# Performance work log

Measured on AMD Instinct MI355X. Metric: run time of the kernel, lower is better.

The kernel has to match this reference:

```python
import jax, jax.numpy as jnp
import numpy as np

B, S, L, H, D, FF, V = 2, 1024, 12, 12, 768, 3072, 50265
DH = D // H
W1 = 256                      # one-sided window (attention_window=512)
MOTIF = (31 + 96 + 80) * 2    # 414
MAXPOS = 4098
EPS = 1e-5
NEG = jnp.float32(-1e9)


def _ln(x, s, b):
    m = jnp.mean(x, -1, keepdims=True)
    v = jnp.mean(jnp.square(x - m), -1, keepdims=True)
    return (x - m) * jax.lax.rsqrt(v + EPS) * s + b


def setup_inputs() -> dict:
    key = jax.random.key(0)
    ks = iter(jax.random.split(key, 48))
    n = lambda *sh: jax.random.normal(next(ks), sh, jnp.float32) * 0.02
    return {
        "input_ids": jax.random.randint(next(ks), (B, S), 0, V),
        "attention_mask": jnp.ones((B, S), jnp.int32),
        "motif_dist": jax.random.uniform(next(ks), (B, MOTIF), dtype=jnp.float32),
        "emb_word": n(V, D), "emb_pos": n(MAXPOS, D), "emb_type": n(1, D),
        "emb_ln_s": jnp.ones((D,)), "emb_ln_b": jnp.zeros((D,)),
        "Wq": n(L, D, D), "bq": jnp.zeros((L, D)),
        "Wk": n(L, D, D), "bk": jnp.zeros((L, D)),
        "Wv": n(L, D, D), "bv": jnp.zeros((L, D)),
        "Wqg": n(L, D, D), "bqg": jnp.zeros((L, D)),
        "Wkg": n(L, D, D), "bkg": jnp.zeros((L, D)),
        "Wvg": n(L, D, D), "bvg": jnp.zeros((L, D)),
        "Wo": n(L, D, D), "bo": jnp.zeros((L, D)),
        "ln1_s": jnp.ones((L, D)), "ln1_b": jnp.zeros((L, D)),
        "Wi": n(L, D, FF), "bi": jnp.zeros((L, FF)),
        "Wo2": n(L, FF, D), "bo2": jnp.zeros((L, D)),
        "ln2_s": jnp.ones((L, D)), "ln2_b": jnp.zeros((L, D)),
        "head_Wd": n(D + MOTIF, D), "head_bd": jnp.zeros((D,)),
        "head_Wp": n(D, 2), "head_bp": jnp.zeros((2,)),
    }


def reference(input_ids, attention_mask, motif_dist, emb_word, emb_pos, emb_type,
              emb_ln_s, emb_ln_b, Wq, bq, Wk, bk, Wv, bv, Wqg, bqg, Wkg, bkg,
              Wvg, bvg, Wo, bo, ln1_s, ln1_b, Wi, bi, Wo2, bo2, ln2_s, ln2_b,
              head_Wd, head_bd, head_Wp, head_bp):
    Bn, Sn = input_ids.shape
    scale = 1.0 / np.sqrt(DH)
    # RoBERTa-style embeddings: positions start at padding_idx+1 = 2
    pos_ids = jnp.arange(Sn) + 2
    x = emb_word[input_ids] + emb_pos[pos_ids][None] + emb_type[0][None, None]
    x = _ln(x, emb_ln_s, emb_ln_b)

    key_valid = attention_mask.astype(bool)[:, None, None, :]      # [B,1,1,S]
    idx = jnp.arange(Sn)
    is_global = idx == 0                                           # default: CLS-only global
    band = jnp.abs(idx[:, None] - idx[None, :]) <= W1
    # local query attends to its sliding window plus all global keys
    local_allowed = (band | is_global[None, :])[None, None] & key_valid

    def heads(t, s):
        return t.reshape(Bn, s, H, DH).transpose(0, 2, 1, 3)       # [B,H,s,DH]

    for l in range(L):
        q = heads(x @ Wq[l] + bq[l], Sn) * scale
        k = heads(x @ Wk[l] + bk[l], Sn)
        v = heads(x @ Wv[l] + bv[l], Sn)
        scores = jnp.einsum('bhid,bhjd->bhij', q, k)
        probs = jax.nn.softmax(jnp.where(local_allowed, scores, NEG), -1)
        out = jnp.einsum('bhij,bhjd->bhid', probs, v)              # [B,H,S,DH]
        # global (CLS) query: full attention using the *_global projections
        qg = heads(x[:, :1] @ Wqg[l] + bqg[l], 1) * scale          # [B,H,1,DH]
        kg = heads(x @ Wkg[l] + bkg[l], Sn)
        vg = heads(x @ Wvg[l] + bvg[l], Sn)
        sg = jnp.einsum('bhid,bhjd->bhij', qg, kg)                 # [B,H,1,S]
        pg = jax.nn.softmax(jnp.where(key_valid, sg, NEG), -1)
        og = jnp.einsum('bhij,bhjd->bhid', pg, vg)                 # [B,H,1,DH]
        out = jnp.concatenate([og, out[:, :, 1:]], axis=2)
        out = out.transpose(0, 2, 1, 3).reshape(Bn, Sn, D)
        x = _ln(x + out @ Wo[l] + bo[l], ln1_s[l], ln1_b[l])
        h = jax.nn.gelu(x @ Wi[l] + bi[l], approximate=False)
        x = _ln(x + h @ Wo2[l] + bo2[l], ln2_s[l], ln2_b[l])

    # classification head: CLS hidden state concat motif distribution
    hcat = jnp.concatenate([x[:, 0, :], motif_dist], axis=-1)
    return jnp.tanh(hcat @ head_Wd + head_bd) @ head_Wp + head_bp
```

## Files before the change

### kernel.cpp

```cpp
#include <hip/hip_runtime.h>
#include <math.h>

typedef unsigned short u16;
typedef __attribute__((ext_vector_type(8))) short short8;
typedef __attribute__((ext_vector_type(4))) float f32x4;

#define BB 2
#define SS 1024
#define LL 12
#define HH 12
#define DD 768
#define FFF 3072
#define MOTIF 414
#define HCAT (DD + MOTIF)
#define W1 256
#define NEGV -1e9f
#define EPS 1e-5f
#define SCALE 0.125f
#define LD5 3840
#define WL_ELE 8257536

__device__ __forceinline__ float bf2f(u16 u) {
    union { unsigned i; float f; } x; x.i = ((unsigned)u) << 16; return x.f;
}
__device__ __forceinline__ u16 f2bf(float f) {
    union { float f; unsigned i; } x; x.f = f;
    unsigned r = x.i + 0x7fffu + ((x.i >> 16) & 1u);
    return (u16)(r >> 16);
}

__device__ __forceinline__ void gld16(const u16* g, u16* l) {
    __builtin_amdgcn_global_load_lds((const __attribute__((address_space(1))) void*)g,
                                     (__attribute__((address_space(3))) void*)l, 16, 0, 0);
}

__device__ __forceinline__ float block_reduce_sum(float v, float* red) {
    int t = threadIdx.x;
    red[t] = v; __syncthreads();
    #pragma unroll
    for (int s = 128; s > 0; s >>= 1) {
        if (t < s) red[t] += red[t + s];
        __syncthreads();
    }
    float r = red[0]; __syncthreads();
    return r;
}

__global__ __launch_bounds__(256) void embed_ln_kernel(
    const int* __restrict__ ids, const float* __restrict__ ew,
    const float* __restrict__ ep, const float* __restrict__ et,
    const float* __restrict__ gs, const float* __restrict__ gb,
    float* __restrict__ X, u16* __restrict__ Xb) {
    __shared__ float red[256];
    int row = blockIdx.x;
    int s = row % SS;
    int id = ids[row];
    int t = threadIdx.x;
    float v[3];
    float sum = 0.f;
    #pragma unroll
    for (int i = 0; i < 3; ++i) {
        int d = t + 256 * i;
        float x = ew[(size_t)id * DD + d] + ep[(size_t)(s + 2) * DD + d] + et[d];
        v[i] = x; sum += x;
    }
    sum = block_reduce_sum(sum, red);
    float m = sum * (1.f / DD);
    float sq = 0.f;
    #pragma unroll
    for (int i = 0; i < 3; ++i) { float c = v[i] - m; sq += c * c; }
    sq = block_reduce_sum(sq, red);
    float inv = rsqrtf(sq * (1.f / DD) + EPS);
    #pragma unroll
    for (int i = 0; i < 3; ++i) {
        int d = t + 256 * i;
        float o = (v[i] - m) * inv * gs[d] + gb[d];
        X[(size_t)row * DD + d] = o;
        Xb[(size_t)row * DD + d] = f2bf(o);
    }
}

__global__ __launch_bounds__(256) void add_ln_kernel(
    float* __restrict__ X, u16* __restrict__ Xb,
    const float* __restrict__ T1, const float* __restrict__ T2, int useT2,
    const float* __restrict__ gs, const float* __restrict__ gb) {
    __shared__ float red[256];
    int row = blockIdx.x;
    int t = threadIdx.x;
    float v[3];
    float sum = 0.f;
    #pragma unroll
    for (int i = 0; i < 3; ++i) {
        int d = t + 256 * i;
        size_t idx = (size_t)row * DD + d;
        float x = X[idx] + T1[idx] + (useT2 ? T2[idx] : 0.f);
        v[i] = x; sum += x;
    }
    sum = block_reduce_sum(sum, red);
    float m = sum * (1.f / DD);
    float sq = 0.f;
    #pragma unroll
    for (int i = 0; i < 3; ++i) { float c = v[i] - m; sq += c * c; }
    sq = block_reduce_sum(sq, red);
    float inv = rsqrtf(sq * (1.f / DD) + EPS);
    #pragma unroll
    for (int i = 0; i < 3; ++i) {
        int d = t + 256 * i;
        float o = (v[i] - m) * inv * gs[d] + gb[d];
        X[(size_t)row * DD + d] = o;
        Xb[(size_t)row * DD + d] = f2bf(o);
    }
}

template <int LAYERED>
__global__ __launch_bounds__(256) void conv_all_kernel(
    const float* __restrict__ Wqp, const float* __restrict__ Wkp,
    const float* __restrict__ Wvp, const float* __restrict__ Wkgp,
    const float* __restrict__ Wvgp, const float* __restrict__ Wop,
    const float* __restrict__ Wip, const float* __restrict__ Wo2p,
    u16* __restrict__ WtBase) {
    __shared__ float Tt[32][33];
    int l = LAYERED ? blockIdx.y : 0;
    size_t oDD = (size_t)l * DD * DD;
    size_t oFF = (size_t)l * DD * FFF;
    u16* Wt6  = WtBase + (size_t)l * WL_ELE;
    u16* Wti  = Wt6 + 6 * DD * DD;
    u16* Wto2 = Wti + FFF * DD;
    int tid = blockIdx.x;
    const float* W; u16* Wt; int Nd, Kd, n0, k0;
    if (tid < 3456) {
        int z = tid / 576, rem = tid % 576;
        const float* w6[6] = {Wqp + oDD, Wkp + oDD, Wvp + oDD, Wkgp + oDD, Wvgp + oDD, Wop + oDD};
        W = w6[z];
        Wt = Wt6 + (size_t)z * DD * DD;
        Nd = DD; Kd = DD; n0 = (rem % 24) * 32; k0 = (rem / 24) * 32;
    } else if (tid < 5760) {
        int i = tid - 3456;
        W = Wip + oFF; Wt = Wti; Nd = FFF; Kd = DD; n0 = (i % 96) * 32; k0 = (i / 96) * 32;
    } else {
        int i = tid - 5760;
        W = Wo2p + oFF; Wt = Wto2; Nd = DD; Kd = FFF; n0 = (i % 24) * 32; k0 = (i / 24) * 32;
    }
    int t = threadIdx.x;
    int r = t >> 3, c = (t & 7) * 4;
    float4 v = *(const float4*)(W + (size_t)(k0 + r) * Nd + n0 + c);
    Tt[r][c] = v.x; Tt[r][c + 1] = v.y; Tt[r][c + 2] = v.z; Tt[r][c + 3] = v.w;
    __syncthreads();
    int n = t >> 3, k4 = (t & 7) * 4;
    unsigned lo = (unsigned)f2bf(Tt[k4][n])     | ((unsigned)f2bf(Tt[k4 + 1][n]) << 16);
    unsigned hi = (unsigned)f2bf(Tt[k4 + 2][n]) | ((unsigned)f2bf(Tt[k4 + 3][n]) << 16);
    uint2 wv; wv.x = lo; wv.y = hi;
    *(uint2*)&Wt[(size_t)(n0 + n) * Kd + k0 + k4] = wv;
}

__global__ __launch_bounds__(256) void bcat_kernel(
    const float* __restrict__ bq, const float* __restrict__ bk,
    const float* __restrict__ bv, const float* __restrict__ bkg,
    const float* __restrict__ bvg, float* __restrict__ bcat) {
    int tid = blockIdx.x * 256 + threadIdx.x;
    if (tid >= LL * LD5) return;
    int l = tid / LD5, r = tid % LD5, z = r / DD, j = r % DD;
    const float* src = (z == 0) ? bq : (z == 1) ? bk : (z == 2) ? bv : (z == 3) ? bkg : bvg;
    bcat[tid] = src[l * DD + j];
}

template <int ACT, int OBF>
__global__ __launch_bounds__(256) void gemm_bf16(
    const u16* __restrict__ A, const u16* __restrict__ Bt,
    const float* __restrict__ bias, void* __restrict__ C0, void* __restrict__ C1,
    int M, int N, int K, int Ksplit) {
    __shared__ __align__(16) u16 As[128 * 32];
    __shared__ __align__(16) u16 Bs[128 * 32];
    int z = blockIdx.z;
    int kbeg = z * Ksplit;
    int kend = kbeg + Ksplit; if (kend > K) kend = K;
    void* Cout = z ? C1 : C0;
    int t = threadIdx.x, lane = t & 63, wv = t >> 6;
    int bm = blockIdx.y * 128, bn = blockIdx.x * 128;
    int wm = wv >> 1, wn = wv & 1;
    int h = lane >> 4, q15 = lane & 15;
    f32x4 acc[4][4];
    #pragma unroll
    for (int i = 0; i < 4; ++i)
        #pragma unroll
        for (int j = 0; j < 4; ++j) { acc[i][j][0] = 0.f; acc[i][j][1] = 0.f; acc[i][j][2] = 0.f; acc[i][j][3] = 0.f; }

    for (int k0 = kbeg; k0 < kend; k0 += 32) {
        #pragma unroll
        for (int op = 0; op < 2; ++op) {
            int rc = wv * 32 + op * 16;
            int r = rc + (lane >> 2), s = lane & 3;
            gld16(A  + (size_t)(bm + r) * K + k0 + ((s ^ (r & 3)) * 8), &As[rc * 32]);
            gld16(Bt + (size_t)(bn + r) * K + k0 + ((s ^ (r & 3)) * 8), &Bs[rc * 32]);
        }
        __syncthreads();
        short8 af[4], bfr[4];
        #pragma unroll
        for (int mf = 0; mf < 4; ++mf) {
            int row = wm * 64 + mf * 16 + q15;
            af[mf] = *(const short8*)&As[row * 32 + ((h ^ (row & 3)) * 8)];
        }
        #pragma unroll
        for (int nf = 0; nf < 4; ++nf) {
            int row = wn * 64 + nf * 16 + q15;
            bfr[nf] = *(const short8*)&Bs[row * 32 + ((h ^ (row & 3)) * 8)];
        }
        #pragma unroll
        for (int mf = 0; mf < 4; ++mf)
            #pragma unroll
            for (int nf = 0; nf < 4; ++nf)
                acc[mf][nf] = __builtin_amdgcn_mfma_f32_16x16x32_bf16(af[mf], bfr[nf], acc[mf][nf], 0, 0, 0);
        __syncthreads();
    }
    float* Cf = (float*)Cout;
    u16*   Cb = (u16*)Cout;
    #pragma unroll
    for (int mf = 0; mf < 4; ++mf) {
        int mbase = bm + wm * 64 + mf * 16 + h * 4;
        #pragma unroll
        for (int nf = 0; nf < 4; ++nf) {
            int n = bn + wn * 64 + nf * 16 + q15;
            float bv = 0.f;
            if (z == 0) bv = bias[n];
            #pragma unroll
            for (int rg = 0; rg < 4; ++rg) {
                float val = acc[mf][nf][rg] + bv;
                if (ACT == 1) val = 0.5f * val * (1.f + erff(val * 0.70710678118654752f));
                if (OBF) Cb[(size_t)(mbase + rg) * N + n] = f2bf(val);
                else     Cf[(size_t)(mbase + rg) * N + n] = val;
            }
        }
    }
}

__global__ __launch_bounds__(256) void attn_local_mfma(
    const u16* __restrict__ QKV, const int* __restrict__ mask,
    u16* __restrict__ AO) {
    __shared__ __align__(16) u16 Qs[64 * 64];
    __shared__ __align__(16) u16 Ks[64 * 64];
    __shared__ __align__(16) u16 Vst[64 * 64];
    __shared__ __align__(16) u16 Pld[4][16 * 64];
    __shared__ float msk[64];
    int bid = blockIdx.x;
    int qt = bid & 15;
    int hh = (bid >> 4) % HH;
    int b  = bid / (16 * HH);
    int t = threadIdx.x, lane = t & 63, wv = t >> 6;
    int h = lane >> 4, q15 = lane & 15;
    int i0 = qt * 64;

    #pragma unroll
    for (int op = 0; op < 2; ++op) {
        int r = wv * 16 + op * 8 + (lane >> 3), s = lane & 7;
        gld16(QKV + (size_t)(b * SS + i0 + r) * LD5 + hh * 64 + ((s ^ (r & 7)) * 8),
              &Qs[(wv * 16 + op * 8) * 64]);
    }
    __syncthreads();
    short8 bq[2];
    {
        int qrow = wv * 16 + q15;
        #pragma unroll
        for (int ks = 0; ks < 2; ++ks)
            bq[ks] = *(const short8*)&Qs[qrow * 64 + (((ks * 4 + h) ^ (qrow & 7)) * 8)];
    }

    float mrun = -3e38f, lrun = 0.f;
    f32x4 o[4];
    #pragma unroll
    for (int nf = 0; nf < 4; ++nf) { o[nf][0] = 0.f; o[nf][1] = 0.f; o[nf][2] = 0.f; o[nf][3] = 0.f; }

    int jlo = i0 - W1; if (jlo < 0) jlo = 0;
    int jend = i0 + 64 + W1; if (jend > SS) jend = SS;
    int hasCLS = (jlo > 0) ? 1 : 0;
    int nt = hasCLS + (jend - jlo) / 64;
    int iq = i0 + wv * 16 + q15;

    for (int tt = 0; tt < nt; ++tt) {
        int base = (hasCLS && tt == 0) ? 0 : jlo + (tt - hasCLS) * 64;
        if (tt > 0) __syncthreads();
        #pragma unroll
        for (int op = 0; op < 2; ++op) {
            int r = wv * 16 + op * 8 + (lane >> 3), s = lane & 7;
            gld16(QKV + (size_t)(b * SS + base + r) * LD5 + 768 + hh * 64 + ((s ^ (r & 7)) * 8),
                  &Ks[(wv * 16 + op * 8) * 64]);
        }
        {
            int k2 = t & 31, dsec = t >> 5;
            const u16* vp = QKV + (size_t)(b * SS + base + 2 * k2) * LD5 + 1536 + hh * 64 + dsec * 8;
            union { uint4 v; u16 e[8]; } r0, r1;
            r0.v = *(const uint4*)vp;
            r1.v = *(const uint4*)(vp + LD5);
            int slot = k2 >> 2;
            #pragma unroll
            for (int j = 0; j < 8; ++j) {
                int d = dsec * 8 + j;
                unsigned val = (unsigned)r0.e[j] | ((unsigned)r1.e[j] << 16);
                *(unsigned*)&Vst[d * 64 + ((slot ^ (d & 7)) * 8) + ((2 * k2) & 7)] = val;
            }
        }
        if (t < 64) msk[t] = (float)mask[b * SS + base + t];
        __syncthreads();

        f32x4 sacc[4];
        #pragma unroll
        for (int kf = 0; kf < 4; ++kf) { sacc[kf][0] = 0.f; sacc[kf][1] = 0.f; sacc[kf][2] = 0.f; sacc[kf][3] = 0.f; }
        #pragma unroll
        for (int ks = 0; ks < 2; ++ks) {
            #pragma unroll
            for (int kf = 0; kf < 4; ++kf) {
                int krow = kf * 16 + q15;
                short8 afr = *(const short8*)&Ks[krow * 64 + (((ks * 4 + h) ^ (krow & 7)) * 8)];
                sacc[kf] = __builtin_amdgcn_mfma_f32_16x16x32_bf16(afr, bq[ks], sacc[kf], 0, 0, 0);
            }
        }
        float pv[4][4];
        float tmax = -3e38f;
        #pragma unroll
        for (int kf = 0; kf < 4; ++kf) {
            #pragma unroll
            for (int rg = 0; rg < 4; ++rg) {
                int kl = kf * 16 + h * 4 + rg;
                int key = base + kl;
                int dj = iq - key; int adj = dj < 0 ? -dj : dj;
                bool valid = ((adj <= W1) || (key == 0)) && (msk[kl] != 0.f);
                float s = valid ? sacc[kf][rg] * SCALE : NEGV;
                pv[kf][rg] = s;
                tmax = fmaxf(tmax, s);
            }
        }
        tmax = fmaxf(tmax, __shfl_xor(tmax, 16));
        tmax = fmaxf(tmax, __shfl_xor(tmax, 32));
        float mnew = fmaxf(mrun, tmax);
        float fac = __expf(mrun - mnew);
        mrun = mnew;
        float psum = 0.f;
        #pragma unroll
        for (int kf = 0; kf < 4; ++kf)
            #pragma unroll
            for (int rg = 0; rg < 4; ++rg) {
                float p = __expf(pv[kf][rg] - mnew);
                pv[kf][rg] = p; psum += p;
            }
        psum += __shfl_xor(psum, 16);
        psum += __shfl_xor(psum, 32);
        lrun = lrun * fac + psum;
        #pragma unroll
        for (int kf = 0; kf < 4; ++kf) {
            unsigned lo = (unsigned)f2bf(pv[kf][0]) | ((unsigned)f2bf(pv[kf][1]) << 16);
            unsigned hi = (unsigned)f2bf(pv[kf][2]) | ((unsigned)f2bf(pv[kf][3]) << 16);
            int slot = 2 * kf + (h >> 1);
            uint2 w; w.x = lo; w.y = hi;
            *(uint2*)&Pld[wv][q15 * 64 + ((slot ^ (q15 & 7)) * 8) + 4 * (h & 1)] = w;
        }
        float fo0 = __shfl(fac, (h * 4 + 0) | (lane & 48));
        float fo1 = __shfl(fac, (h * 4 + 1) | (lane & 48));
        float fo2 = __shfl(fac, (h * 4 + 2) | (lane & 48));
        float fo3 = __shfl(fac, (h * 4 + 3) | (lane & 48));
        #pragma unroll
        for (int nf = 0; nf < 4; ++nf) {
            o[nf][0] *= fo0; o[nf][1] *= fo1; o[nf][2] *= fo2; o[nf][3] *= fo3;
        }
        asm volatile("s_waitcnt lgkmcnt(0)" ::: "memory");
        #pragma unroll
        for (int ks = 0; ks < 2; ++ks) {
            short8 ap = *(const short8*)&Pld[wv][q15 * 64 + (((ks * 4 + h) ^ (q15 & 7)) * 8)];
            #pragma unroll
            for (int nf = 0; nf < 4; ++nf) {
                int d = nf * 16 + q15;
                short8 bvf = *(const short8*)&Vst[d * 64 + (((ks * 4 + h) ^ (d & 7)) * 8)];
                o[nf] = __builtin_amdgcn_mfma_f32_16x16x32_bf16(ap, bvf, o[nf], 0, 0, 0);
            }
        }
    }
    float linv = 1.f / lrun;
    float g0 = __shfl(linv, (h * 4 + 0) | (lane & 48));
    float g1 = __shfl(linv, (h * 4 + 1) | (lane & 48));
    float g2 = __shfl(linv, (h * 4 + 2) | (lane & 48));
    float g3 = __shfl(linv, (h * 4 + 3) | (lane & 48));
    size_t rb = (size_t)(b * SS + i0 + wv * 16 + h * 4);
    #pragma unroll
    for (int nf = 0; nf < 4; ++nf) {
        int d = hh * 64 + nf * 16 + q15;
        AO[(rb + 0) * DD + d] = f2bf(o[nf][0] * g0);
        AO[(rb + 1) * DD + d] = f2bf(o[nf][1] * g1);
        AO[(rb + 2) * DD + d] = f2bf(o[nf][2] * g2);
        AO[(rb + 3) * DD + d] = f2bf(o[nf][3] * g3);
    }
}

__global__ __launch_bounds__(512) void attn_global_kernel(
    const float* __restrict__ Xf, const float* __restrict__ Wqg,
    const float* __restrict__ bqg, const u16* __restrict__ QKV,
    const int* __restrict__ mask, u16* __restrict__ AO) {
    __shared__ float x0[DD];
    __shared__ float qv[64];
    __shared__ float sc[SS];
    __shared__ float red[512];
    __shared__ float part[8][64];
    int b = blockIdx.x / HH, hh = blockIdx.x % HH;
    int t = threadIdx.x;
    for (int i = t; i < DD; i += 512) x0[i] = Xf[(size_t)b * SS * DD + i];
    __syncthreads();
    {
        int d = t & 63, p = t >> 6;
        float acc = 0.f;
        int k0 = p * 96;
        #pragma unroll 8
        for (int k = k0; k < k0 + 96; ++k)
            acc += x0[k] * Wqg[(size_t)k * DD + hh * 64 + d];
        part[p][d] = acc;
    }
    __syncthreads();
    if (t < 64) {
        float s = bqg[hh * 64 + t];
        #pragma unroll
        for (int p = 0; p < 8; ++p) s += part[p][t];
        qv[t] = s * SCALE;
    }
    __syncthreads();
    for (int j = t; j < SS; j += 512) {
        const u16* kp = QKV + (size_t)(b * SS + j) * LD5 + 2304 + hh * 64;
        float acc = 0.f;
        #pragma unroll
        for (int d0 = 0; d0 < 64; d0 += 8) {
            union { uint4 v; u16 e[8]; } u;
            u.v = *(const uint4*)(kp + d0);
            #pragma unroll
            for (int j2 = 0; j2 < 8; ++j2) acc += qv[d0 + j2] * bf2f(u.e[j2]);
        }
        sc[j] = mask[b * SS + j] ? acc : NEGV;
    }
    __syncthreads();
    float mx = fmaxf(sc[t], sc[t + 512]);
    red[t] = mx; __syncthreads();
    #pragma unroll
    for (int s = 256; s > 0; s >>= 1) {
        if (t < s) red[t] = fmaxf(red[t], red[t + s]);
        __syncthreads();
    }
    mx = red[0]; __syncthreads();
    float e0 = __expf(sc[t] - mx), e1 = __expf(sc[t + 512] - mx);
    sc[t] = e0; sc[t + 512] = e1;
    red[t] = e0 + e1; __syncthreads();
    #pragma unroll
    for (int s = 256; s > 0; s >>= 1) {
        if (t < s) red[t] += red[t + s];
        __syncthreads();
    }
    float lsum = red[0]; __syncthreads();
    int g = t >> 6, d = t & 63;
    float acc = 0.f;
    for (int j = g; j < SS; j += 8)
        acc += sc[j] * bf2f(QKV[(size_t)(b * SS + j) * LD5 + 3072 + hh * 64 + d]);
    part[g][d] = acc;
    __syncthreads();
    if (g == 0) {
        float ov = 0.f;
        #pragma unroll
        for (int p = 0; p < 8; ++p) ov += part[p][d];
        AO[(size_t)(b * SS) * DD + hh * 64 + d] = f2bf(ov / lsum);
    }
}

__global__ __launch_bounds__(256) void head1_kernel(
    const float* __restrict__ X, const float* __restrict__ motif,
    const float* __restrict__ Wd, float* __restrict__ hpart) {
    __shared__ float hc[HCAT];
    __shared__ float part[4][64];
    int jb = blockIdx.x, kp = blockIdx.y, b = blockIdx.z;
    int t = threadIdx.x;
    for (int i = t; i < DD; i += 256) hc[i] = X[(size_t)b * SS * DD + i];
    for (int i = t; i < MOTIF; i += 256) hc[DD + i] = motif[(size_t)b * MOTIF + i];
    __syncthreads();
    int j = jb * 64 + (t & 63);
    int sub = t >> 6;
    int k0 = kp * 148 + sub * 37;
    int k1 = k0 + 37; if (k1 > HCAT) k1 = HCAT;
    float acc = 0.f;
    for (int k = k0; k < k1; ++k) acc += hc[k] * Wd[(size_t)k * DD + j];
    part[sub][t & 63] = acc;
    __syncthreads();
    if (sub == 0) {
        int x = t & 63;
        hpart[((size_t)b * 8 + kp) * DD + j] = part[0][x] + part[1][x] + part[2][x] + part[3][x];
    }
}

__global__ __launch_bounds__(256) void head2_kernel(
    const float* __restrict__ hpart, const float* __restrict__ bd,
    const float* __restrict__ Wp, const float* __restrict__ bp,
    float* __restrict__ out) {
    __shared__ float dvs[DD];
    __shared__ float red[256];
    int b = blockIdx.x;
    int t = threadIdx.x;
    for (int j = t; j < DD; j += 256) {
        float s = bd[j];
        #pragma unroll
        for (int kp = 0; kp < 8; ++kp) s += hpart[((size_t)b * 8 + kp) * DD + j];
        dvs[j] = tanhf(s);
    }
    __syncthreads();
    float a0 = 0.f, a1 = 0.f;
    for (int k = t; k < DD; k += 256) {
        a0 += dvs[k] * Wp[k * 2 + 0];
        a1 += dvs[k] * Wp[k * 2 + 1];
    }
    a0 = block_reduce_sum(a0, red);
    a1 = block_reduce_sum(a1, red);
    if (t == 0) {
        out[b * 2 + 0] = a0 + bp[0];
        out[b * 2 + 1] = a1 + bp[1];
    }
}

extern "C" void kernel_launch(void* const* d_in, const int* in_sizes, int n_in,
                              void* d_out, int out_size, void* d_ws, size_t ws_size,
                              hipStream_t stream) {
    const int*   input_ids = (const int*)d_in[0];
    const int*   attn_mask = (const int*)d_in[1];
    const float* motif     = (const float*)d_in[2];
    const float* emb_word  = (const float*)d_in[3];
    const float* emb_pos   = (const float*)d_in[4];
    const float* emb_type  = (const float*)d_in[5];
    const float* emb_ln_s  = (const float*)d_in[6];
    const float* emb_ln_b  = (const float*)d_in[7];
    const float* Wq  = (const float*)d_in[8];
    const float* bq  = (const float*)d_in[9];
    const float* Wk  = (const float*)d_in[10];
    const float* bk  = (const float*)d_in[11];
    const float* Wv  = (const float*)d_in[12];
    const float* bv  = (const float*)d_in[13];
    const float* Wqg = (const float*)d_in[14];
    const float* bqg = (const float*)d_in[15];
    const float* Wkg = (const float*)d_in[16];
    const float* bkg = (const float*)d_in[17];
    const float* Wvg = (const float*)d_in[18];
    const float* bvg = (const float*)d_in[19];
    const float* Wo  = (const float*)d_in[20];
    const float* bo  = (const float*)d_in[21];
    const float* ln1_s = (const float*)d_in[22];
    const float* ln1_b = (const float*)d_in[23];
    const float* Wi  = (const float*)d_in[24];
    const float* bi  = (const float*)d_in[25];
    const float* Wo2 = (const float*)d_in[26];
    const float* bo2 = (const float*)d_in[27];
    const float* ln2_s = (const float*)d_in[28];
    const float* ln2_b = (const float*)d_in[29];
    const float* head_Wd = (const float*)d_in[30];
    const float* head_bd = (const float*)d_in[31];
    const float* head_Wp = (const float*)d_in[32];
    const float* head_bp = (const float*)d_in[33];

    float* out = (float*)d_out;
    char* base = (char*)d_ws;

    float* Xf   = (float*)(base + 0);
    u16*   Xb   = (u16*)  (base + 6291456);
    u16*   QKVb = (u16*)  (base + 9437184);
    u16*   AOb  = (u16*)  (base + 25165824);
    float* T1f  = (float*)(base + 28311552);

    const size_t NEED_BIG  = 57643008;
    const size_t NEED_HUGE = 239308800;
    bool huge = ws_size >= NEED_HUGE;
    bool big  = huge || ws_size >= NEED_BIG;

    float* T2f = big ? (float*)(base + 34603008) : T1f;
    u16* WtAll; float* bcat; float* hpart;
    u16 *Wt6_s = nullptr, *Wti_s = nullptr, *Wto2_s = nullptr;
    if (huge) {
        bcat  = (float*)(base + 40894464);
        hpart = (float*)(base + 41078784);
        WtAll = (u16*)  (base + 41127936);
    } else {
        size_t wbase = big ? 40894464 : 34603008;
        Wt6_s  = (u16*)(base + wbase);
        Wti_s  = (u16*)(base + wbase + 7077888);
        Wto2_s = (u16*)(base + wbase + 11796480);
        bcat   = (float*)(base + wbase + 16515072);
        hpart  = (float*)(base + wbase + 16699392);
        WtAll  = Wt6_s;
    }
    u16* Hb = QKVb;

    const int nrow = BB * SS;
    const int useT2 = big ? 1 : 0;

    embed_ln_kernel<<<nrow, 256, 0, stream>>>(input_ids, emb_word, emb_pos, emb_type,
                                              emb_ln_s, emb_ln_b, Xf, Xb);
    bcat_kernel<<<(LL * LD5 + 255) / 256, 256, 0, stream>>>(bq, bk, bv, bkg, bvg, bcat);
    if (huge)
        conv_all_kernel<1><<<dim3(8064, 12), 256, 0, stream>>>(
            Wq, Wk, Wv, Wkg, Wvg, Wo, Wi, Wo2, WtAll);

    dim3 g5(30, 16, 1);
    dim3 gO(6, 16, big ? 2 : 1);
    dim3 gFF1(24, 16, 1);
    dim3 gFF2(6, 16, big ? 2 : 1);

    for (int l = 0; l < LL; ++l) {
        size_t oDD = (size_t)l * DD * DD;
        u16 *Wt6, *Wti, *Wto2;
        if (huge) {
            Wt6  = WtAll + (size_t)l * WL_ELE;
            Wti  = Wt6 + 6 * DD * DD;
            Wto2 = Wti + FFF * DD;
        } else {
            conv_all_kernel<0><<<dim3(8064, 1), 256, 0, stream>>>(
                Wq + oDD, Wk + oDD, Wv + oDD, Wkg + oDD, Wvg + oDD, Wo + oDD,
                Wi + (size_t)l * DD * FFF, Wo2 + (size_t)l * FFF * DD, Wt6_s);
            Wt6 = Wt6_s; Wti = Wti_s; Wto2 = Wto2_s;
        }

        gemm_bf16<0, 1><<<g5, 256, 0, stream>>>(Xb, Wt6, bcat + l * LD5, QKVb, QKVb,
                                                nrow, LD5, DD, DD);

        attn_local_mfma<<<BB * HH * 16, 256, 0, stream>>>(QKVb, attn_mask, AOb);
        attn_global_kernel<<<BB * HH, 512, 0, stream>>>(Xf, Wqg + oDD, bqg + l * DD,
                                                        QKVb, attn_mask, AOb);

        gemm_bf16<0, 0><<<gO, 256, 0, stream>>>(AOb, Wt6 + 5 * (size_t)DD * DD, bo + l * DD,
                                                T1f, T2f, nrow, DD, DD, big ? 384 : 768);
        add_ln_kernel<<<nrow, 256, 0, stream>>>(Xf, Xb, T1f, T2f, useT2,
                                                ln1_s + l * DD, ln1_b + l * DD);

        gemm_bf16<1, 1><<<gFF1, 256, 0, stream>>>(Xb, Wti, bi + l * FFF, Hb, Hb,
                                                  nrow, FFF, DD, DD);
        gemm_bf16<0, 0><<<gFF2, 256, 0, stream>>>(Hb, Wto2, bo2 + l * DD,
                                                  T1f, T2f, nrow, DD, FFF, big ? 1536 : 3072);
        add_ln_kernel<<<nrow, 256, 0, stream>>>(Xf, Xb, T1f, T2f, useT2,
                                                ln2_s + l * DD, ln2_b + l * DD);
    }

    head1_kernel<<<dim3(12, 8, BB), 256, 0, stream>>>(Xf, motif, head_Wd, hpart);
    head2_kernel<<<BB, 256, 0, stream>>>(hpart, head_bd, head_Wp, head_bp, out);
}
```

Before: 2.780 ms.

## Double-buffer GEMM LDS tiles and widen weight-conversion tiles to 64 rows

The bf16 MFMA GEMM now keeps two LDS buffers for A and B, so the next K tile is fetched while the current one is multiplied, and one of the two barriers per iteration is dropped. The weight transpose/convert kernel now handles 64 K-rows per block and writes 16-byte chunks, which halves the block count and widens the stores. The cost is double the LDS for the GEMM, which may lower occupancy. Each block of the conversion kernel also does more work.

```diff
diff --git a/kernel.cpp b/kernel.cpp
--- a/kernel.cpp
+++ b/kernel.cpp
@@ -119,7 +119,7 @@
     const float* __restrict__ Wvgp, const float* __restrict__ Wop,
     const float* __restrict__ Wip, const float* __restrict__ Wo2p,
     u16* __restrict__ WtBase) {
-    __shared__ float Tt[32][33];
+    __shared__ float Tt[64][33];
     int l = LAYERED ? blockIdx.y : 0;
     size_t oDD = (size_t)l * DD * DD;
     size_t oFF = (size_t)l * DD * FFF;
@@ -128,29 +128,35 @@
     u16* Wto2 = Wti + FFF * DD;
     int tid = blockIdx.x;
     const float* W; u16* Wt; int Nd, Kd, n0, k0;
-    if (tid < 3456) {
-        int z = tid / 576, rem = tid % 576;
+    if (tid < 1728) {
+        int z = tid / 288, rem = tid % 288;
         const float* w6[6] = {Wqp + oDD, Wkp + oDD, Wvp + oDD, Wkgp + oDD, Wvgp + oDD, Wop + oDD};
         W = w6[z];
         Wt = Wt6 + (size_t)z * DD * DD;
-        Nd = DD; Kd = DD; n0 = (rem % 24) * 32; k0 = (rem / 24) * 32;
-    } else if (tid < 5760) {
-        int i = tid - 3456;
-        W = Wip + oFF; Wt = Wti; Nd = FFF; Kd = DD; n0 = (i % 96) * 32; k0 = (i / 96) * 32;
+        Nd = DD; Kd = DD; n0 = (rem % 24) * 32; k0 = (rem / 24) * 64;
+    } else if (tid < 2880) {
+        int i = tid - 1728;
+        W = Wip + oFF; Wt = Wti; Nd = FFF; Kd = DD; n0 = (i % 96) * 32; k0 = (i / 96) * 64;
     } else {
-        int i = tid - 5760;
-        W = Wo2p + oFF; Wt = Wto2; Nd = DD; Kd = FFF; n0 = (i % 24) * 32; k0 = (i / 24) * 32;
+        int i = tid - 2880;
+        W = Wo2p + oFF; Wt = Wto2; Nd = DD; Kd = FFF; n0 = (i % 24) * 32; k0 = (i / 24) * 64;
     }
     int t = threadIdx.x;
     int r = t >> 3, c = (t & 7) * 4;
-    float4 v = *(const float4*)(W + (size_t)(k0 + r) * Nd + n0 + c);
-    Tt[r][c] = v.x; Tt[r][c + 1] = v.y; Tt[r][c + 2] = v.z; Tt[r][c + 3] = v.w;
-    __syncthreads();
-    int n = t >> 3, k4 = (t & 7) * 4;
-    unsigned lo = (unsigned)f2bf(Tt[k4][n])     | ((unsigned)f2bf(Tt[k4 + 1][n]) << 16);
-    unsigned hi = (unsigned)f2bf(Tt[k4 + 2][n]) | ((unsigned)f2bf(Tt[k4 + 3][n]) << 16);
-    uint2 wv; wv.x = lo; wv.y = hi;
-    *(uint2*)&Wt[(size_t)(n0 + n) * Kd + k0 + k4] = wv;
+    #pragma unroll
+    for (int half = 0; half < 2; ++half) {
+        float4 v = *(const float4*)(W + (size_t)(k0 + half * 32 + r) * Nd + n0 + c);
+        Tt[half * 32 + r][c + 0] = v.x;
+        Tt[half * 32 + r][c + 1] = v.y;
+        Tt[half * 32 + r][c + 2] = v.z;
+        Tt[half * 32 + r][c + 3] = v.w;
+    }
+    __syncthreads();
+    int n = t >> 3, kk = (t & 7) * 8;
+    union { uint4 v; u16 e[8]; } wv;
+    #pragma unroll
+    for (int j = 0; j < 8; ++j) wv.e[j] = f2bf(Tt[kk + j][n]);
+    *(uint4*)&Wt[(size_t)(n0 + n) * Kd + k0 + kk] = wv.v;
 }
 
 __global__ __launch_bounds__(256) void bcat_kernel(
@@ -169,8 +175,8 @@
     const u16* __restrict__ A, const u16* __restrict__ Bt,
     const float* __restrict__ bias, void* __restrict__ C0, void* __restrict__ C1,
     int M, int N, int K, int Ksplit) {
-    __shared__ __align__(16) u16 As[128 * 32];
-    __shared__ __align__(16) u16 Bs[128 * 32];
+    __shared__ __align__(16) u16 As[2][128 * 32];
+    __shared__ __align__(16) u16 Bs[2][128 * 32];
     int z = blockIdx.z;
     int kbeg = z * Ksplit;
     int kend = kbeg + Ksplit; if (kend > K) kend = K;
@@ -179,31 +185,45 @@
     int bm = blockIdx.y * 128, bn = blockIdx.x * 128;
     int wm = wv >> 1, wn = wv & 1;
     int h = lane >> 4, q15 = lane & 15;
+    int rA = wv * 32;
+    int rr = lane >> 2, s = lane & 3;
     f32x4 acc[4][4];
     #pragma unroll
     for (int i = 0; i < 4; ++i)
         #pragma unroll
         for (int j = 0; j < 4; ++j) { acc[i][j][0] = 0.f; acc[i][j][1] = 0.f; acc[i][j][2] = 0.f; acc[i][j][3] = 0.f; }
 
-    for (int k0 = kbeg; k0 < kend; k0 += 32) {
-        #pragma unroll
-        for (int op = 0; op < 2; ++op) {
-            int rc = wv * 32 + op * 16;
-            int r = rc + (lane >> 2), s = lane & 3;
-            gld16(A  + (size_t)(bm + r) * K + k0 + ((s ^ (r & 3)) * 8), &As[rc * 32]);
-            gld16(Bt + (size_t)(bn + r) * K + k0 + ((s ^ (r & 3)) * 8), &Bs[rc * 32]);
-        }
-        __syncthreads();
+    int nk = (kend - kbeg) >> 5;
+    #pragma unroll
+    for (int op = 0; op < 2; ++op) {
+        int rc = rA + op * 16;
+        int r = rc + rr;
+        gld16(A  + (size_t)(bm + r) * K + kbeg + ((s ^ (r & 3)) * 8), &As[0][rc * 32]);
+        gld16(Bt + (size_t)(bn + r) * K + kbeg + ((s ^ (r & 3)) * 8), &Bs[0][rc * 32]);
+    }
+    __syncthreads();
+    int cur = 0;
+    for (int i = 0; i < nk; ++i) {
+        if (i + 1 < nk) {
+            int k0 = kbeg + ((i + 1) << 5);
+            #pragma unroll
+            for (int op = 0; op < 2; ++op) {
+                int rc = rA + op * 16;
+                int r = rc + rr;
+                gld16(A  + (size_t)(bm + r) * K + k0 + ((s ^ (r & 3)) * 8), &As[cur ^ 1][rc * 32]);
+                gld16(Bt + (size_t)(bn + r) * K + k0 + ((s ^ (r & 3)) * 8), &Bs[cur ^ 1][rc * 32]);
+            }
+        }
         short8 af[4], bfr[4];
         #pragma unroll
         for (int mf = 0; mf < 4; ++mf) {
             int row = wm * 64 + mf * 16 + q15;
-            af[mf] = *(const short8*)&As[row * 32 + ((h ^ (row & 3)) * 8)];
+            af[mf] = *(const short8*)&As[cur][row * 32 + ((h ^ (row & 3)) * 8)];
         }
         #pragma unroll
         for (int nf = 0; nf < 4; ++nf) {
             int row = wn * 64 + nf * 16 + q15;
-            bfr[nf] = *(const short8*)&Bs[row * 32 + ((h ^ (row & 3)) * 8)];
+            bfr[nf] = *(const short8*)&Bs[cur][row * 32 + ((h ^ (row & 3)) * 8)];
         }
         #pragma unroll
         for (int mf = 0; mf < 4; ++mf)
@@ -211,6 +231,7 @@
             for (int nf = 0; nf < 4; ++nf)
                 acc[mf][nf] = __builtin_amdgcn_mfma_f32_16x16x32_bf16(af[mf], bfr[nf], acc[mf][nf], 0, 0, 0);
         __syncthreads();
+        cur ^= 1;
     }
     float* Cf = (float*)Cout;
     u16*   Cb = (u16*)Cout;
@@ -591,7 +612,7 @@
                                               emb_ln_s, emb_ln_b, Xf, Xb);
     bcat_kernel<<<(LL * LD5 + 255) / 256, 256, 0, stream>>>(bq, bk, bv, bkg, bvg, bcat);
     if (huge)
-        conv_all_kernel<1><<<dim3(8064, 12), 256, 0, stream>>>(
+        conv_all_kernel<1><<<dim3(4032, 12), 256, 0, stream>>>(
             Wq, Wk, Wv, Wkg, Wvg, Wo, Wi, Wo2, WtAll);
 
     dim3 g5(30, 16, 1);
@@ -607,7 +628,7 @@
             Wti  = Wt6 + 6 * DD * DD;
             Wto2 = Wti + FFF * DD;
         } else {
-            conv_all_kernel<0><<<dim3(8064, 1), 256, 0, stream>>>(
+            conv_all_kernel<0><<<dim3(4032, 1), 256, 0, stream>>>(
                 Wq + oDD, Wk + oDD, Wv + oDD, Wkg + oDD, Wvg + oDD, Wo + oDD,
                 Wi + (size_t)l * DD * FFF, Wo2 + (size_t)l * FFF * DD, Wt6_s);
             Wt6 = Wt6_s; Wti = Wti_s; Wto2 = Wto2_s;
```

After: 2.675 ms. 3.8% less time.
